# Kernel tuning notes

Measured on AMD Instinct MI355X. Metric: run time of the kernel, lower is better.

The kernel has to match this reference:

```python
import jax, jax.numpy as jnp
import numpy as np

# 18000 genes, 50 SNPs per gene (900k SNPs total), each gene block has layersize 16
B, G, K, L = 32, 18000, 50, 16
N_SNPS = G * K


def setup_inputs() -> dict:
    key = jax.random.key(0)
    k1, k2, k3, k4, k5 = jax.random.split(key, 5)
    x = jax.random.normal(k1, (B, N_SNPS), dtype=jnp.float32)
    # gene_scaling_layer: diagonal 1x1 blocks -> per-SNP scale + bias, Identity activation
    scale_w = jax.random.normal(k2, (N_SNPS,), dtype=jnp.float32)
    scale_b = jax.random.normal(k3, (N_SNPS,), dtype=jnp.float32) * 0.01
    # block-sparse weights: one [1, L] weight per (snp, gene) edge, grouped per gene -> [G, K, L]
    W = jax.random.normal(k4, (G, K, L), dtype=jnp.float32) * (1.0 / np.sqrt(K))
    b = jax.random.normal(k5, (G, L), dtype=jnp.float32) * 0.01
    # SNP indices feeding each gene (consecutive assignment, as in the torch construction loop)
    snp_index = jnp.arange(N_SNPS, dtype=jnp.int32).reshape(G, K)
    return {"x": x, "scale_w": scale_w, "scale_b": scale_b, "W": W, "b": b, "snp_index": snp_index}


def reference(x, scale_w, scale_b, W, b, snp_index):
    # scaling layer (diagonal block-sparse linear, identity activation, no dropout at eval)
    xs = x * scale_w + scale_b                      # [B, N_SNPS]
    # gather SNP features per gene block (irregular access pattern)
    xg = xs[:, snp_index]                           # [B, G, K]
    # block-sparse GEMM: each gene sums its incident SNP edge weights
    out = jnp.einsum("bgk,gkl->bgl", xg, W) + b     # [B, G, L]
    out = jax.nn.relu(out)
    return out.reshape(out.shape[0], -1)            # [B, G*L]
```

## Files before the change

### kernel.cpp

```cpp
#include <hip/hip_runtime.h>


#define B_ 32
#define G_ 18000
#define K_ 50
#define L_ 16
#define NS_ (G_ * K_)
#define GPB 4
#define THREADS_ (GPB * 64)

__global__ __launch_bounds__(THREADS_, 2)
void gene_model_kernel(const float* __restrict__ x,
                       const float* __restrict__ sw,
                       const float* __restrict__ sb,
                       const float* __restrict__ W,
                       const float* __restrict__ bias,
                       const int*   __restrict__ sidx,
                       float*       __restrict__ out) {
  const int wave = __builtin_amdgcn_readfirstlane((int)(threadIdx.x >> 6));
  const int lane = (int)(threadIdx.x & 63);
  const int g    = (int)blockIdx.x * GPB + wave;
  const int b    = lane & 31;
  const int l0   = (lane >> 5) * 8;

  const float* __restrict__ Wg   = W + (size_t)g * (K_ * L_) + l0;
  const float* __restrict__ xrow = x + (size_t)b * NS_;
  const int*   __restrict__ idxg = sidx + g * K_;

  float acc[8];
  {
    const float4 bv0 = *reinterpret_cast<const float4*>(bias + (size_t)g * L_ + l0);
    const float4 bv1 = *reinterpret_cast<const float4*>(bias + (size_t)g * L_ + l0 + 4);
    acc[0] = bv0.x; acc[1] = bv0.y; acc[2] = bv0.z; acc[3] = bv0.w;
    acc[4] = bv1.x; acc[5] = bv1.y; acc[6] = bv1.z; acc[7] = bv1.w;
  }

#pragma unroll 5
  for (int k = 0; k < K_; ++k) {
    const int   idx = idxg[k];
    const float xs  = fmaf(xrow[idx], sw[idx], sb[idx]);
    const float4 w0 = *reinterpret_cast<const float4*>(Wg + k * L_);
    const float4 w1 = *reinterpret_cast<const float4*>(Wg + k * L_ + 4);
    acc[0] = fmaf(xs, w0.x, acc[0]);
    acc[1] = fmaf(xs, w0.y, acc[1]);
    acc[2] = fmaf(xs, w0.z, acc[2]);
    acc[3] = fmaf(xs, w0.w, acc[3]);
    acc[4] = fmaf(xs, w1.x, acc[4]);
    acc[5] = fmaf(xs, w1.y, acc[5]);
    acc[6] = fmaf(xs, w1.z, acc[6]);
    acc[7] = fmaf(xs, w1.w, acc[7]);
  }

  float4 o0, o1;
  o0.x = fmaxf(acc[0], 0.f); o0.y = fmaxf(acc[1], 0.f);
  o0.z = fmaxf(acc[2], 0.f); o0.w = fmaxf(acc[3], 0.f);
  o1.x = fmaxf(acc[4], 0.f); o1.y = fmaxf(acc[5], 0.f);
  o1.z = fmaxf(acc[6], 0.f); o1.w = fmaxf(acc[7], 0.f);

  float* op = out + (size_t)b * (G_ * L_) + (size_t)g * L_ + l0;
  *reinterpret_cast<float4*>(op)     = o0;
  *reinterpret_cast<float4*>(op + 4) = o1;
}

extern "C" void kernel_launch(void* const* d_in, const int* in_sizes, int n_in,
                              void* d_out, int out_size, void* d_ws, size_t ws_size,
                              hipStream_t stream) {
  const float* x    = (const float*)d_in[0];
  const float* sw   = (const float*)d_in[1];
  const float* sb   = (const float*)d_in[2];
  const float* W    = (const float*)d_in[3];
  const float* bias = (const float*)d_in[4];
  const int*   sidx = (const int*)d_in[5];
  float*       out  = (float*)d_out;

  dim3 grid(G_ / GPB);
  dim3 block(THREADS_);
  gene_model_kernel<<<grid, block, 0, stream>>>(x, sw, sb, W, bias, sidx, out);
}
```

Measured before the change: 359.7 us.

## Stage scaled gathered SNP tile in LDS before per-gene accumulation

Each block now loads the 4 genes' SNP indices, scales and biases into shared memory once. It then cooperatively gathers and scales the 32x200 activation tile into LDS, with consecutive threads covering consecutive columns, before the FMA loop reads from LDS. Previously each lane did strided per-row global reads of x, sw and sb, and the two lanes sharing a batch row repeated the same loads. This adds two barriers, about 27KB of LDS per block, and a higher occupancy hint in launch bounds.

New measurement: 291.7 us. -18.9%, faster.

```diff
diff --git a/kernel.cpp b/kernel.cpp
--- a/kernel.cpp
+++ b/kernel.cpp
@@ -6,10 +6,13 @@
 #define K_ 50
 #define L_ 16
 #define NS_ (G_ * K_)
-#define GPB 4
-#define THREADS_ (GPB * 64)
+#define GT 4
+#define COLS (GT * K_)
+#define Q_ (COLS / 4)
+#define XS_STRIDE 204
+#define THREADS_ 256
 
-__global__ __launch_bounds__(THREADS_, 2)
+__global__ __launch_bounds__(THREADS_, 4)
 void gene_model_kernel(const float* __restrict__ x,
                        const float* __restrict__ sw,
                        const float* __restrict__ sb,
@@ -17,15 +20,46 @@
                        const float* __restrict__ bias,
                        const int*   __restrict__ sidx,
                        float*       __restrict__ out) {
-  const int wave = __builtin_amdgcn_readfirstlane((int)(threadIdx.x >> 6));
-  const int lane = (int)(threadIdx.x & 63);
-  const int g    = (int)blockIdx.x * GPB + wave;
+  __shared__ float xs_lds[B_ * XS_STRIDE];
+  __shared__ float swc[COLS];
+  __shared__ float sbc[COLS];
+  __shared__ int   idxc[COLS];
+
+  const int tid = (int)threadIdx.x;
+  const int g0  = (int)blockIdx.x * GT;
+
+  if (tid < COLS) {
+    const int idx = sidx[g0 * K_ + tid];
+    idxc[tid] = idx;
+    swc[tid]  = sw[idx];
+    sbc[tid]  = sb[idx];
+  }
+  __syncthreads();
+
+  for (int i = tid; i < B_ * Q_; i += THREADS_) {
+    const int r  = i / Q_;
+    const int c4 = (i - r * Q_) * 4;
+    const float* __restrict__ xr = x + (size_t)r * NS_;
+    const int4   iv = *reinterpret_cast<const int4*>(&idxc[c4]);
+    const float4 sv = *reinterpret_cast<const float4*>(&swc[c4]);
+    const float4 bv = *reinterpret_cast<const float4*>(&sbc[c4]);
+    float4 v;
+    v.x = fmaf(xr[iv.x], sv.x, bv.x);
+    v.y = fmaf(xr[iv.y], sv.y, bv.y);
+    v.z = fmaf(xr[iv.z], sv.z, bv.z);
+    v.w = fmaf(xr[iv.w], sv.w, bv.w);
+    *reinterpret_cast<float4*>(&xs_lds[r * XS_STRIDE + c4]) = v;
+  }
+  __syncthreads();
+
+  const int wave = __builtin_amdgcn_readfirstlane(tid >> 6);
+  const int lane = tid & 63;
+  const int g    = g0 + wave;
   const int b    = lane & 31;
   const int l0   = (lane >> 5) * 8;
 
-  const float* __restrict__ Wg   = W + (size_t)g * (K_ * L_) + l0;
-  const float* __restrict__ xrow = x + (size_t)b * NS_;
-  const int*   __restrict__ idxg = sidx + g * K_;
+  const float* __restrict__ Wg  = W + (size_t)g * (K_ * L_) + l0;
+  const float* __restrict__ xsp = &xs_lds[b * XS_STRIDE + wave * K_];
 
   float acc[8];
   {
@@ -37,18 +71,17 @@
 
 #pragma unroll 5
   for (int k = 0; k < K_; ++k) {
-    const int   idx = idxg[k];
-    const float xs  = fmaf(xrow[idx], sw[idx], sb[idx]);
+    const float  xv = xsp[k];
     const float4 w0 = *reinterpret_cast<const float4*>(Wg + k * L_);
     const float4 w1 = *reinterpret_cast<const float4*>(Wg + k * L_ + 4);
-    acc[0] = fmaf(xs, w0.x, acc[0]);
-    acc[1] = fmaf(xs, w0.y, acc[1]);
-    acc[2] = fmaf(xs, w0.z, acc[2]);
-    acc[3] = fmaf(xs, w0.w, acc[3]);
-    acc[4] = fmaf(xs, w1.x, acc[4]);
-    acc[5] = fmaf(xs, w1.y, acc[5]);
-    acc[6] = fmaf(xs, w1.z, acc[6]);
-    acc[7] = fmaf(xs, w1.w, acc[7]);
+    acc[0] = fmaf(xv, w0.x, acc[0]);
+    acc[1] = fmaf(xv, w0.y, acc[1]);
+    acc[2] = fmaf(xv, w0.z, acc[2]);
+    acc[3] = fmaf(xv, w0.w, acc[3]);
+    acc[4] = fmaf(xv, w1.x, acc[4]);
+    acc[5] = fmaf(xv, w1.y, acc[5]);
+    acc[6] = fmaf(xv, w1.z, acc[6]);
+    acc[7] = fmaf(xv, w1.w, acc[7]);
   }
 
   float4 o0, o1;
@@ -73,7 +106,7 @@
   const int*   sidx = (const int*)d_in[5];
   float*       out  = (float*)d_out;
 
-  dim3 grid(G_ / GPB);
+  dim3 grid(G_ / GT);
   dim3 block(THREADS_);
   gene_model_kernel<<<grid, block, 0, stream>>>(x, sw, sb, W, bias, sidx, out);
 }
```
